# Kernel optimization log

Measured on AMD Instinct MI355X. Metric: run time of the kernel, lower is better.

Reference implementation:

```python
import jax, jax.numpy as jnp
import numpy as np

N = 100_000      # nodes
E = 1_600_000    # edges (avg degree 16)
IN = 512         # in_feats
HID = 4          # hidden_feats (forced equal to num_heads=4 by the mean(h,2) in forward)
H1 = 4           # heads in layer 1
OUT = 128        # out_feats
NEG_SLOPE = 0.2  # DGL GATConv leaky_relu default


def setup_inputs() -> dict:
    key = jax.random.key(0)
    ks = jax.random.split(key, 12)
    nfeats = jax.random.normal(ks[0], (N, IN), jnp.float32)
    efeats = jax.random.normal(ks[1], (E, 8), jnp.float32)  # unused by the module
    src = jax.random.randint(ks[2], (E,), 0, N, dtype=jnp.int32)
    dst = jax.random.randint(ks[3], (E,), 0, N, dtype=jnp.int32)
    # layer 1 params (in=IN, heads=H1, per-head out=HID)
    fc1_w = jax.random.normal(ks[4], (IN, H1 * HID), jnp.float32) / np.sqrt(IN)
    attn_l1 = jax.random.normal(ks[5], (H1, HID), jnp.float32) / np.sqrt(HID)
    attn_r1 = jax.random.normal(ks[6], (H1, HID), jnp.float32) / np.sqrt(HID)
    bias1 = jnp.zeros((H1 * HID,), jnp.float32)
    # layer 2 params (in=H1=4 after mean over feature dim, heads=1, out=OUT)
    fc2_w = jax.random.normal(ks[7], (HID, 1 * OUT), jnp.float32) / np.sqrt(HID)
    attn_l2 = jax.random.normal(ks[8], (1, OUT), jnp.float32) / np.sqrt(OUT)
    attn_r2 = jax.random.normal(ks[9], (1, OUT), jnp.float32) / np.sqrt(OUT)
    bias2 = jnp.zeros((OUT,), jnp.float32)
    return {"nfeats": nfeats, "efeats": efeats, "src": src, "dst": dst,
            "fc1_w": fc1_w, "attn_l1": attn_l1, "attn_r1": attn_r1, "bias1": bias1,
            "fc2_w": fc2_w, "attn_l2": attn_l2, "attn_r2": attn_r2, "bias2": bias2}


def gat_layer(x, src, dst, fc_w, attn_l, attn_r, bias, heads, d_out):
    # projection: (N, in) -> (N, H, D)
    h = (x @ fc_w).reshape(-1, heads, d_out)
    el = jnp.einsum('nhd,hd->nh', h, attn_l)   # (N, H)
    er = jnp.einsum('nhd,hd->nh', h, attn_r)
    e = jax.nn.leaky_relu(el[src] + er[dst], NEG_SLOPE)  # (E, H)
    # segment softmax over incoming edges of each dst node
    m = jax.lax.stop_gradient(jax.ops.segment_max(e, dst, num_segments=N))
    ex = jnp.exp(e - m[dst])
    denom = jax.ops.segment_sum(ex, dst, num_segments=N)
    alpha = ex / denom[dst]                    # (E, H)
    msg = alpha[:, :, None] * h[src]           # (E, H, D)
    rst = jax.ops.segment_sum(msg, dst, num_segments=N)  # (N, H, D)
    return rst + bias.reshape(1, heads, d_out)


def reference(nfeats, efeats, src, dst, fc1_w, attn_l1, attn_r1, bias1,
              fc2_w, attn_l2, attn_r2, bias2):
    h = gat_layer(nfeats, src, dst, fc1_w, attn_l1, attn_r1, bias1, H1, HID)  # (N,4,4)
    h = jnp.mean(h, axis=2)        # faithful to th.mean(h, 2): mean over per-head feat dim -> (N,4)
    h = jax.nn.relu(h)
    h = gat_layer(h, src, dst, fc2_w, attn_l2, attn_r2, bias2, 1, OUT)        # (N,1,OUT)
    return h.reshape(N, OUT)       # flatten(1)
```

## Files before the change

kernel.cpp:

```cpp
#include <hip/hip_runtime.h>
#include <math.h>

#define IN_F 512
#define OUTF 128
#define NEG_SLOPE 0.2f

typedef __attribute__((ext_vector_type(8))) short bf16x8;
typedef __attribute__((ext_vector_type(4))) float f32x4;

#define P1T 256
#define XP 136
#define NKS 16
#define BPSH 8192

#define NPB 128
#define NBMAX 784
#define EPB 8192
#define SRCMASK 0x1FFFF
#define CAP 2944

#define BP_BYTES (BPSH * 2)
#define XS_BYTES (4 * 16 * XP * 2)
#define SMEM_A   (BP_BYTES + XS_BYTES)

__device__ __forceinline__ unsigned pkbf(float a, float b) {
  unsigned ua = __float_as_uint(a); ua += 0x7FFF + ((ua >> 16) & 1);
  unsigned ub = __float_as_uint(b); ub += 0x7FFF + ((ub >> 16) & 1);
  return (ua >> 16) | (ub & 0xFFFF0000u);
}

__global__ void k_prep(const float* __restrict__ fc1, const float* __restrict__ al1,
                       const float* __restrict__ ar1, const float* __restrict__ fc2,
                       const float* __restrict__ al2, const float* __restrict__ ar2,
                       unsigned short* __restrict__ Bp,
                       float* __restrict__ w2al, float* __restrict__ w2ar,
                       int* __restrict__ bucketCursor) {
  __shared__ float wlds[IN_F * 12];
  int t = threadIdx.x;
  if (blockIdx.x == 0) {
    int k = t;
#pragma unroll
    for (int h = 0; h < 4; ++h) {
      float wl = 0.f, wr = 0.f, wb = 0.f;
#pragma unroll
      for (int j = 0; j < 4; ++j) {
        float wv = fc1[k * 16 + h * 4 + j];
        wl = fmaf(wv, al1[h * 4 + j], wl);
        wr = fmaf(wv, ar1[h * 4 + j], wr);
        wb += wv;
      }
      wlds[k * 12 + h] = wl;
      wlds[k * 12 + 4 + h] = wr;
      wlds[k * 12 + 8 + h] = 0.25f * wb;
    }
    __syncthreads();
    for (int item = t; item < NKS * 64; item += 512) {
      int s = item >> 6, l = item & 63;
      int col = l & 15;
      int kb = s * 32 + ((l >> 4) * 8);
      unsigned hi[4];
#pragma unroll
      for (int p = 0; p < 4; ++p) {
        float w0 = 0.f, w1 = 0.f;
        if (col < 12) {
          w0 = wlds[(kb + 2 * p) * 12 + col];
          w1 = wlds[(kb + 2 * p + 1) * 12 + col];
        }
        hi[p] = pkbf(w0, w1);
      }
      *(uint4*)&Bp[item * 8] = make_uint4(hi[0], hi[1], hi[2], hi[3]);
    }
  } else {
    if (t < 8) {
      int h = t >> 1;
      const float* a = (t & 1) ? ar2 : al2;
      float s = 0.f;
#pragma unroll 16
      for (int c = 0; c < OUTF; ++c) s += fc2[h * OUTF + c] * a[c];
      if (t & 1) w2ar[h] = s; else w2al[h] = s;
    }
    for (int i = t; i < NBMAX; i += 512) bucketCursor[i] = 0;
  }
}

__global__ __launch_bounds__(P1T) void k_A(
    const float* __restrict__ x, const unsigned short* __restrict__ Bp,
    float* __restrict__ pk1, float* __restrict__ er1, int n,
    const int* __restrict__ src, const int* __restrict__ dst,
    int* __restrict__ bucketCursor, unsigned* __restrict__ ep, int e,
    int binBlocks, int projBlocks)
{
  __shared__ __align__(16) char smem[SMEM_A];
  const int t = threadIdx.x;

  if ((int)blockIdx.x < binBlocks) {
    int* hist = (int*)smem;
    int* base = hist + NBMAX;
    int* lcur = base + NBMAX;
    const int bb = blockIdx.x;
    for (int i = t; i < NBMAX; i += P1T) hist[i] = 0;
    __syncthreads();
    int blockBase = bb * EPB;
#pragma unroll
    for (int i = 0; i < EPB / P1T; ++i) {
      int idx = blockBase + t + i * P1T;
      if (idx < e) atomicAdd(&hist[dst[idx] >> 7], 1);
    }
    __syncthreads();
    for (int i = t; i < NBMAX; i += P1T) {
      if (hist[i] > 0) base[i] = atomicAdd(&bucketCursor[i], hist[i]);
      lcur[i] = 0;
    }
    __syncthreads();
#pragma unroll
    for (int i = 0; i < EPB / P1T; ++i) {
      int idx = blockBase + t + i * P1T;
      if (idx < e) {
        int d = dst[idx];
        int b = d >> 7;
        int off = base[b] + atomicAdd(&lcur[b], 1);
        if (off < CAP)
          ep[(size_t)b * CAP + off] = (unsigned)src[idx] | ((unsigned)(d & (NPB - 1)) << 17);
      }
    }
  } else {
    const int pb = blockIdx.x - binBlocks;
    const int lane = t & 63;
    const int wv = t >> 6;
    const bf16x8* Bfrag = (const bf16x8*)smem;
    short* xsw = (short*)(smem + BP_BYTES) + wv * (16 * XP);

    for (int i = t; i < NKS * 64; i += P1T)
      ((uint4*)smem)[i] = ((const uint4*)Bp)[i];
    __syncthreads();

    const int totalWaves = projBlocks * 4;
    const int rtMax = (n + 15) >> 4;
    for (int rt = pb * 4 + wv; rt < rtMax; rt += totalWaves) {
      const int wrow = rt * 16;
      const float* __restrict__ xr = x + (size_t)wrow * IN_F;
      f32x4 acc = {0.f, 0.f, 0.f, 0.f};

      float4 st[8];
#pragma unroll
      for (int i = 0; i < 8; ++i) {
        int f = lane + i * 64;
        int r = f >> 5, c4 = (f & 31) * 4;
        st[i] = (wrow + r < n) ? *(const float4*)&xr[(size_t)r * IN_F + c4]
                               : make_float4(0.f, 0.f, 0.f, 0.f);
      }

      for (int kt = 0; kt < 4; ++kt) {
#pragma unroll
        for (int i = 0; i < 8; ++i) {
          int f = lane + i * 64;
          int r = f >> 5, c4 = (f & 31) * 4;
          uint2 pv; pv.x = pkbf(st[i].x, st[i].y); pv.y = pkbf(st[i].z, st[i].w);
          *(uint2*)&xsw[r * XP + c4] = pv;
        }
        if (kt < 3) {
          int kb = (kt + 1) * 128;
#pragma unroll
          for (int i = 0; i < 8; ++i) {
            int f = lane + i * 64;
            int r = f >> 5, c4 = (f & 31) * 4;
            st[i] = (wrow + r < n) ? *(const float4*)&xr[(size_t)r * IN_F + kb + c4]
                                   : make_float4(0.f, 0.f, 0.f, 0.f);
          }
        }
        asm volatile("s_waitcnt lgkmcnt(0)" ::: "memory");
        __builtin_amdgcn_sched_barrier(0);
#pragma unroll
        for (int ks = 0; ks < 4; ++ks) {
          bf16x8 a = *(const bf16x8*)&xsw[(lane & 15) * XP + ks * 32 + ((lane >> 4) * 8)];
          bf16x8 bh = Bfrag[(kt * 4 + ks) * 64 + lane];
          acc = __builtin_amdgcn_mfma_f32_16x16x32_bf16(a, bh, acc, 0, 0, 0);
        }
      }

      int col = lane & 15;
      int rbase = wrow + ((lane >> 4) * 4);
#pragma unroll
      for (int i = 0; i < 4; ++i) {
        int row = rbase + i;
        if (row < n) {
          float v = acc[i];
          if (col < 4)       pk1[(size_t)row * 8 + col] = v;
          else if (col < 8)  er1[(size_t)row * 4 + (col - 4)] = v;
          else if (col < 12) pk1[(size_t)row * 8 + 4 + (col - 8)] = v;
        }
      }
    }
  }
}

__global__ __launch_bounds__(256) void k_B(
    const unsigned* __restrict__ ep, const int* __restrict__ bucketCursor,
    unsigned* __restrict__ ep2, int* __restrict__ nodeBeg, int* __restrict__ nodeEnd,
    const float* __restrict__ pk1, const float* __restrict__ er1,
    const float* __restrict__ bias1,
    const float* __restrict__ w2al, const float* __restrict__ w2ar,
    float* __restrict__ pk2, float* __restrict__ er2, int n)
{
  __shared__ int cnt[NPB];
  __shared__ int scn[NPB];
  __shared__ int cur[NPB];
  __shared__ unsigned lbuf[CAP];
  int t = threadIdx.x;
  int b = blockIdx.x;
  int nodeBase = b * NPB;
  int m = bucketCursor[b];
  if (m > CAP) m = CAP;
  const unsigned* __restrict__ in = ep + (size_t)b * CAP;
  if (t < NPB) cnt[t] = 0;
  __syncthreads();
  for (int j = t; j < m; j += 256) atomicAdd(&cnt[in[j] >> 17], 1);
  __syncthreads();
  if (t < NPB) scn[t] = cnt[t];
  __syncthreads();
  for (int off = 1; off < NPB; off <<= 1) {
    int v = (t < NPB && t >= off) ? scn[t - off] : 0;
    __syncthreads();
    if (t < NPB) scn[t] += v;
    __syncthreads();
  }
  if (t < NPB) {
    int excl = scn[t] - cnt[t];
    int node = nodeBase + t;
    if (node < n) {
      nodeBeg[node] = b * CAP + excl;
      nodeEnd[node] = b * CAP + excl + cnt[t];
    }
    cur[t] = excl;
  }
  __syncthreads();
  for (int j = t; j < m; j += 256) {
    unsigned p = in[j];
    int pos = atomicAdd(&cur[p >> 17], 1);
    lbuf[pos] = p & SRCMASK;
  }
  __syncthreads();
  for (int i = t; i < m; i += 256) ep2[(size_t)b * CAP + i] = lbuf[i];

#pragma unroll
  for (int half = 0; half < 2; ++half) {
    int w = t + half * 256;
    int i = w >> 2, h = w & 3;
    int node = nodeBase + i;
    bool active = node < n;
    float v = 0.f;
    if (active) {
      int beg = scn[i] - cnt[i], end = scn[i];
      float ern = er1[(size_t)node * 4 + h];
      float den = 0.f, num = 0.f;
      for (int j = beg; j < end; ++j) {
        int s = (int)lbuf[j];
        float el = pk1[(size_t)s * 8 + h];
        float hb = pk1[(size_t)s * 8 + 4 + h];
        float eh = el + ern;
        eh = (eh > 0.f) ? eh : NEG_SLOPE * eh;
        float wg = __expf(eh);
        den += wg;
        num = fmaf(wg, hb, num);
      }
      float mb = 0.25f * (bias1[h*4] + bias1[h*4+1] + bias1[h*4+2] + bias1[h*4+3]);
      v = (end > beg) ? num / den : 0.f;
      v += mb;
      v = (v > 0.f) ? v : 0.f;
    }
    float pl = v * w2al[h];
    float pr = v * w2ar[h];
    pl += __shfl_xor(pl, 1); pl += __shfl_xor(pl, 2);
    pr += __shfl_xor(pr, 1); pr += __shfl_xor(pr, 2);
    if (active) {
      pk2[(size_t)node * 8 + h] = v;
      if (h == 0) { pk2[(size_t)node * 8 + 4] = pl; er2[node] = pr; }
    }
  }
}

__global__ __launch_bounds__(256) void k_bagg2(
    const unsigned* __restrict__ ep2, const int* __restrict__ nodeBeg,
    const int* __restrict__ nodeEnd,
    const float* __restrict__ pk2, const float* __restrict__ er2,
    const float* __restrict__ w2, const float* __restrict__ bias2,
    float* __restrict__ out, int n)
{
  __shared__ float gacc[256 * 4];
  __shared__ float w2s[4 * OUTF];
  __shared__ float b2s[OUTF];
  int t = threadIdx.x;
  int nodeBase = blockIdx.x * 256;
  int nn = nodeBase + t;
  for (int i = t; i < 4 * OUTF; i += 256) w2s[i] = w2[i];
  if (t < OUTF) b2s[t] = bias2[t];
  float g0 = 0.f, g1 = 0.f, g2 = 0.f, g3 = 0.f;
  if (nn < n) {
    int beg = nodeBeg[nn], end = nodeEnd[nn];
    float ern = er2[nn];
    float den = 0.f;
    for (int j = beg; j < end; ++j) {
      int s = (int)ep2[j];
      const float* __restrict__ ps = &pk2[(size_t)s * 8];
      float4 hv = *(const float4*)ps;
      float e = ps[4] + ern;
      e = (e > 0.f) ? e : NEG_SLOPE * e;
      float w = __expf(e);
      den += w;
      g0 = fmaf(w, hv.x, g0); g1 = fmaf(w, hv.y, g1);
      g2 = fmaf(w, hv.z, g2); g3 = fmaf(w, hv.w, g3);
    }
    float inv = (end > beg) ? 1.0f / den : 0.f;
    g0 *= inv; g1 *= inv; g2 *= inv; g3 *= inv;
  }
  gacc[t * 4 + 0] = g0; gacc[t * 4 + 1] = g1;
  gacc[t * 4 + 2] = g2; gacc[t * 4 + 3] = g3;
  __syncthreads();
  for (int idx = t; idx < 256 * (OUTF / 2); idx += 256) {
    int i = idx >> 6;
    int node = nodeBase + i;
    if (node >= n) continue;
    int c = (idx & 63) * 2;
    float gx = gacc[i*4], gy = gacc[i*4+1], gz = gacc[i*4+2], gw = gacc[i*4+3];
    float2 o;
    o.x = gx*w2s[c]   + gy*w2s[OUTF+c]   + gz*w2s[2*OUTF+c]   + gw*w2s[3*OUTF+c]   + b2s[c];
    o.y = gx*w2s[c+1] + gy*w2s[OUTF+c+1] + gz*w2s[2*OUTF+c+1] + gw*w2s[3*OUTF+c+1] + b2s[c+1];
    *(float2*)&out[(size_t)node * OUTF + c] = o;
  }
}

extern "C" void kernel_launch(void* const* d_in, const int* in_sizes, int n_in,
                              void* d_out, int out_size, void* d_ws, size_t ws_size,
                              hipStream_t stream) {
  const float* nfeats = (const float*)d_in[0];
  const int*   srcp   = (const int*)d_in[2];
  const int*   dstp   = (const int*)d_in[3];
  const float* fc1    = (const float*)d_in[4];
  const float* al1    = (const float*)d_in[5];
  const float* ar1    = (const float*)d_in[6];
  const float* bias1  = (const float*)d_in[7];
  const float* fc2    = (const float*)d_in[8];
  const float* al2    = (const float*)d_in[9];
  const float* ar2    = (const float*)d_in[10];
  const float* bias2  = (const float*)d_in[11];

  const int N = in_sizes[0] / IN_F;
  const int E = in_sizes[2];
  const int NB = (N + NPB - 1) / NPB;

  float* ws   = (float*)d_ws;
  float* pk1  = ws;
  float* er1  = pk1 + (size_t)8 * N;
  float* pk2  = er1 + (size_t)4 * N;
  float* er2  = pk2 + (size_t)8 * N;
  float* w2al = er2 + N;
  float* w2ar = w2al + 4;
  unsigned short* Bp = (unsigned short*)(w2ar + 4);
  int* bucketCursor = (int*)(Bp + BPSH);
  int* nodeBeg      = bucketCursor + NBMAX;
  int* nodeEnd      = nodeBeg + N;
  unsigned* ep      = (unsigned*)(nodeEnd + N);
  unsigned* ep2     = ep + (size_t)NB * CAP;

  const int binBlocks = (E + EPB - 1) / EPB;
  const int projBlocks = 391;

  k_prep<<<2, 512, 0, stream>>>(fc1, al1, ar1, fc2, al2, ar2,
                                Bp, w2al, w2ar, bucketCursor);
  k_A<<<binBlocks + projBlocks, P1T, 0, stream>>>(nfeats, Bp, pk1, er1, N,
                                                  srcp, dstp, bucketCursor, ep, E,
                                                  binBlocks, projBlocks);
  k_B<<<NB, 256, 0, stream>>>(ep, bucketCursor, ep2, nodeBeg, nodeEnd,
                              pk1, er1, bias1, w2al, w2ar, pk2, er2, N);
  k_bagg2<<<(N + 255) / 256, 256, 0, stream>>>(ep2, nodeBeg, nodeEnd, pk2, er2,
                                               fc2, bias2, (float*)d_out, N);
}
```

Baseline: 134.5 us.

## Stream projection input tiles via global_load_lds ring buffer with B fragments in registers

```diff
diff --git a/kernel.cpp b/kernel.cpp
--- a/kernel.cpp
+++ b/kernel.cpp
@@ -7,11 +7,16 @@
 
 typedef __attribute__((ext_vector_type(8))) short bf16x8;
 typedef __attribute__((ext_vector_type(4))) float f32x4;
+typedef __attribute__((ext_vector_type(4))) unsigned u32x4;
+typedef const __attribute__((address_space(1))) void gvoid;
+typedef __attribute__((address_space(3))) void lvoid;
 
 #define P1T 256
-#define XP 136
 #define NKS 16
 #define BPSH 8192
+#define TW 64
+#define TILE_B (16 * TW * 4)
+#define RING 3
 
 #define NPB 128
 #define NBMAX 784
@@ -19,14 +24,31 @@
 #define SRCMASK 0x1FFFF
 #define CAP 2944
 
-#define BP_BYTES (BPSH * 2)
-#define XS_BYTES (4 * 16 * XP * 2)
-#define SMEM_A   (BP_BYTES + XS_BYTES)
+#define SMEM_A (4 * RING * TILE_B)
 
 __device__ __forceinline__ unsigned pkbf(float a, float b) {
   unsigned ua = __float_as_uint(a); ua += 0x7FFF + ((ua >> 16) & 1);
   unsigned ub = __float_as_uint(b); ub += 0x7FFF + ((ub >> 16) & 1);
   return (ua >> 16) | (ub & 0xFFFF0000u);
+}
+
+#define VMCNT8() do { asm volatile("s_waitcnt vmcnt(8)" ::: "memory"); \
+                      __builtin_amdgcn_sched_barrier(0); } while (0)
+#define VMCNT4() do { asm volatile("s_waitcnt vmcnt(4)" ::: "memory"); \
+                      __builtin_amdgcn_sched_barrier(0); } while (0)
+#define VMCNT0() do { asm volatile("s_waitcnt vmcnt(0)" ::: "memory"); \
+                      __builtin_amdgcn_sched_barrier(0); } while (0)
+
+__device__ __forceinline__ void issue_tile(const float* __restrict__ x, int wrow,
+                                           int kbase, char* lbase, int lane) {
+#pragma unroll
+  for (int i = 0; i < 4; ++i) {
+    int f = lane + i * 64;
+    int r = f >> 4, c16 = f & 15;
+    int srcu = c16 ^ (r & 7);
+    const float* g = x + (size_t)(wrow + r) * IN_F + kbase + srcu * 4;
+    __builtin_amdgcn_global_load_lds((gvoid*)g, (lvoid*)(lbase + i * 1024), 16, 0, 0);
+  }
 }
 
 __global__ void k_prep(const float* __restrict__ fc1, const float* __restrict__ al1,
@@ -127,59 +149,48 @@
     const int pb = blockIdx.x - binBlocks;
     const int lane = t & 63;
     const int wv = t >> 6;
-    const bf16x8* Bfrag = (const bf16x8*)smem;
-    short* xsw = (short*)(smem + BP_BYTES) + wv * (16 * XP);
-
-    for (int i = t; i < NKS * 64; i += P1T)
-      ((uint4*)smem)[i] = ((const uint4*)Bp)[i];
-    __syncthreads();
-
+    char* ring = smem + (size_t)wv * (RING * TILE_B);
+
+    bf16x8 Breg[NKS];
+#pragma unroll
+    for (int i = 0; i < NKS; ++i)
+      Breg[i] = *(const bf16x8*)&Bp[(i * 64 + lane) * 8];
+
+    const int R = lane & 15;
+    const int g = lane >> 4;
+    const int sw = R & 7;
     const int totalWaves = projBlocks * 4;
     const int rtMax = (n + 15) >> 4;
+
     for (int rt = pb * 4 + wv; rt < rtMax; rt += totalWaves) {
       const int wrow = rt * 16;
-      const float* __restrict__ xr = x + (size_t)wrow * IN_F;
       f32x4 acc = {0.f, 0.f, 0.f, 0.f};
 
-      float4 st[8];
-#pragma unroll
-      for (int i = 0; i < 8; ++i) {
-        int f = lane + i * 64;
-        int r = f >> 5, c4 = (f & 31) * 4;
-        st[i] = (wrow + r < n) ? *(const float4*)&xr[(size_t)r * IN_F + c4]
-                               : make_float4(0.f, 0.f, 0.f, 0.f);
-      }
-
-      for (int kt = 0; kt < 4; ++kt) {
-#pragma unroll
-        for (int i = 0; i < 8; ++i) {
-          int f = lane + i * 64;
-          int r = f >> 5, c4 = (f & 31) * 4;
-          uint2 pv; pv.x = pkbf(st[i].x, st[i].y); pv.y = pkbf(st[i].z, st[i].w);
-          *(uint2*)&xsw[r * XP + c4] = pv;
+      issue_tile(x, wrow, 0, ring + 0 * TILE_B, lane);
+      issue_tile(x, wrow, TW, ring + 1 * TILE_B, lane);
+
+#pragma unroll
+      for (int T = 0; T < 8; ++T) {
+        if (T < 6) issue_tile(x, wrow, (T + 2) * TW, ring + ((T + 2) % 3) * TILE_B, lane);
+        if (T < 6)      { VMCNT8(); }
+        else if (T == 6){ VMCNT4(); }
+        else            { VMCNT0(); }
+        const char* lb = ring + (T % 3) * TILE_B;
+#pragma unroll
+        for (int ks = 0; ks < 2; ++ks) {
+          int j16 = ks * 8 + g * 2;
+          float4 a0 = *(const float4*)(lb + R * 256 + ((j16) ^ sw) * 16);
+          float4 a1 = *(const float4*)(lb + R * 256 + ((j16 + 1) ^ sw) * 16);
+          u32x4 au = {pkbf(a0.x, a0.y), pkbf(a0.z, a0.w),
+                      pkbf(a1.x, a1.y), pkbf(a1.z, a1.w)};
+          union { u32x4 u; bf16x8 v; } cvt; cvt.u = au;
+          acc = __builtin_amdgcn_mfma_f32_16x16x32_bf16(cvt.v, Breg[T * 2 + ks],
+                                                        acc, 0, 0, 0);
         }
-        if (kt < 3) {
-          int kb = (kt + 1) * 128;
-#pragma unroll
-          for (int i = 0; i < 8; ++i) {
-            int f = lane + i * 64;
-            int r = f >> 5, c4 = (f & 31) * 4;
-            st[i] = (wrow + r < n) ? *(const float4*)&xr[(size_t)r * IN_F + kb + c4]
-                                   : make_float4(0.f, 0.f, 0.f, 0.f);
-          }
-        }
-        asm volatile("s_waitcnt lgkmcnt(0)" ::: "memory");
-        __builtin_amdgcn_sched_barrier(0);
-#pragma unroll
-        for (int ks = 0; ks < 4; ++ks) {
-          bf16x8 a = *(const bf16x8*)&xsw[(lane & 15) * XP + ks * 32 + ((lane >> 4) * 8)];
-          bf16x8 bh = Bfrag[(kt * 4 + ks) * 64 + lane];
-          acc = __builtin_amdgcn_mfma_f32_16x16x32_bf16(a, bh, acc, 0, 0, 0);
-        }
       }
 
       int col = lane & 15;
-      int rbase = wrow + ((lane >> 4) * 4);
+      int rbase = wrow + (g * 4);
 #pragma unroll
       for (int i = 0; i < 4; ++i) {
         int row = rbase + i;
@@ -363,7 +374,7 @@
   unsigned* ep2     = ep + (size_t)NB * CAP;
 
   const int binBlocks = (E + EPB - 1) / EPB;
-  const int projBlocks = 391;
+  const int projBlocks = 572;
 
   k_prep<<<2, 512, 0, stream>>>(fc1, al1, ar1, fc2, al2, ar2,
                                 Bp, w2al, w2ar, bucketCursor);
```

Result: no change. 133.1 us (median of 2 runs) (-1.0%).
